# Kernel optimization log

Measured on AMD Instinct MI355X. Metric: run time of the kernel, lower is better.

## Reference

```python
import jax, jax.numpy as jnp
import numpy as np

N_LAYERS = 4
D_MODEL = 64        # 8*8 hardcoded in source
D_STATE = 128
D_CONV = 4
EXPAND = 2
HEADDIM = 64        # Mamba2Simple default
D_INNER = EXPAND * D_MODEL            # 128
NHEADS = D_INNER // HEADDIM           # 2
NGROUPS = 1
D_IN_PROJ = 2 * D_INNER + 2 * NGROUPS * D_STATE + NHEADS   # 514
CONV_DIM = D_INNER + 2 * NGROUPS * D_STATE                 # 384
EPS = 1e-5
B_SZ, SEQ = 8, 4096


def setup_inputs() -> dict:
    key = jax.random.key(0)
    ks = jax.random.split(key, 8)
    s = 0.02
    x = jax.random.normal(ks[0], (B_SZ, SEQ, D_MODEL), jnp.float32)
    in_proj_w = jax.random.normal(ks[1], (N_LAYERS, D_IN_PROJ, D_MODEL), jnp.float32) * s
    conv_w = jax.random.normal(ks[2], (N_LAYERS, CONV_DIM, 1, D_CONV), jnp.float32) * 0.2
    conv_b = jnp.zeros((N_LAYERS, CONV_DIM), jnp.float32)
    # dt_bias ~ inverse-softplus of small dt values
    dt_bias = jax.random.uniform(ks[3], (N_LAYERS, NHEADS), jnp.float32, -4.0, 0.0)
    A_log = jnp.log(jax.random.uniform(ks[4], (N_LAYERS, NHEADS), jnp.float32, 1.0, 16.0))
    D = jnp.ones((N_LAYERS, NHEADS), jnp.float32)
    norm_w = jnp.ones((N_LAYERS, D_INNER), jnp.float32)
    out_proj_w = jax.random.normal(ks[5], (N_LAYERS, D_MODEL, D_INNER), jnp.float32) * s
    return {"x": x, "in_proj_w": in_proj_w, "conv_w": conv_w, "conv_b": conv_b,
            "dt_bias": dt_bias, "A_log": A_log, "D": D, "norm_w": norm_w,
            "out_proj_w": out_proj_w}


def _ssm(xh, dt, A, Bm, Cm):
    """Selective-scan SSM. xh:(B,L,H,P) dt:(B,L,H) A:(H,) Bm,Cm:(B,L,S) -> (B,L,H,P)"""
    dA = jnp.exp(dt * A)  # (B,L,H)

    def step(h, inp):
        dA_t, dt_t, x_t, B_t, C_t = inp
        # h: (B,H,P,S)
        h = h * dA_t[:, :, None, None] + (dt_t[:, :, None] * x_t)[..., None] * B_t[:, None, None, :]
        y = jnp.einsum('bhps,bs->bhp', h, C_t)
        return h, y

    b = xh.shape[0]
    h0 = jnp.zeros((b, NHEADS, HEADDIM, D_STATE), xh.dtype)
    xs = (jnp.moveaxis(dA, 1, 0), jnp.moveaxis(dt, 1, 0), jnp.moveaxis(xh, 1, 0),
          jnp.moveaxis(Bm, 1, 0), jnp.moveaxis(Cm, 1, 0))
    _, ys = jax.lax.scan(step, h0, xs)
    return jnp.moveaxis(ys, 0, 1)


def _layer(x, p):
    in_w, cw, cb, dtb, Alog, Dp, nw, ow = p
    zxbcdt = x @ in_w.T                                   # (B,L,514)
    z = zxbcdt[..., :D_INNER]
    xBC = zxbcdt[..., D_INNER:D_INNER + CONV_DIM]
    dt = jax.nn.softplus(zxbcdt[..., -NHEADS:] + dtb)     # (B,L,H)
    # causal depthwise conv over sequence
    xc = jnp.moveaxis(xBC, -1, 1)                         # (B,C,L)
    xc = jax.lax.conv_general_dilated(xc, cw, (1,), [(D_CONV - 1, 0)],
                                      dimension_numbers=('NCH', 'OIH', 'NCH'),
                                      feature_group_count=CONV_DIM)
    xBC = jax.nn.silu(jnp.moveaxis(xc + cb[None, :, None], 1, -1))
    xs = xBC[..., :D_INNER]
    Bm = xBC[..., D_INNER:D_INNER + D_STATE]
    Cm = xBC[..., D_INNER + D_STATE:]
    xh = xs.reshape(xs.shape[0], xs.shape[1], NHEADS, HEADDIM)
    A = -jnp.exp(Alog)                                    # (H,)
    y = _ssm(xh, dt, A, Bm, Cm) + Dp[None, None, :, None] * xh
    y = y.reshape(y.shape[0], y.shape[1], D_INNER)
    # gated RMSNorm (norm_before_gate=False): rmsnorm(y * silu(z)) * w
    y = y * jax.nn.silu(z)
    y = y * jax.lax.rsqrt(jnp.mean(y * y, axis=-1, keepdims=True) + EPS) * nw
    return y @ ow.T


def reference(x, in_proj_w, conv_w, conv_b, dt_bias, A_log, D, norm_w, out_proj_w):
    def body(xc, p):
        return _layer(xc, p) + xc, None
    out, _ = jax.lax.scan(body, x, (in_proj_w, conv_w, conv_b, dt_bias, A_log, D, norm_w, out_proj_w))
    return out
```

## Files before the change

### kernel.cpp

```cpp
#include <hip/hip_runtime.h>
#include <math.h>

#define B_SZ 8
#define SEQ  4096
#define DM   64
#define DI   128
#define NH   2
#define HD   64
#define DS   128
#define DIP  514
#define ZW   512
#define CD   384
#define QC   64
#define NC   64
#define NR   (B_SZ*SEQ)
#define WPAD 576

typedef __attribute__((ext_vector_type(8))) short bf16x8;
typedef __attribute__((ext_vector_type(4))) float f32x4;

__device__ __forceinline__ unsigned short f2bf(float f) {
    union { float f; unsigned int u; } x; x.f = f;
    unsigned int r = x.u + 0x7fffu + ((x.u >> 16) & 1u);
    return (unsigned short)(r >> 16);
}
__device__ __forceinline__ float bf2f(unsigned short h) {
    union { unsigned int u; float f; } x; x.u = ((unsigned int)h) << 16;
    return x.f;
}
__device__ __forceinline__ bf16x8 fragld(const unsigned short* base, int r0, int k0, int ld) {
    int l = threadIdx.x & 63;
    return *(const bf16x8*)(base + (ptrdiff_t)(r0 + (l & 15)) * ld + k0 + (l >> 4) * 8);
}

__global__ __launch_bounds__(256) void k_wcvt(const float* __restrict__ in_w,
                                              const float* __restrict__ out_w,
                                              unsigned short* __restrict__ Wb,
                                              unsigned short* __restrict__ OWb) {
    int idx = blockIdx.x * 256 + threadIdx.x;
    if (idx < 4 * WPAD * 64) {
        int l = idx / (WPAD * 64), r = idx % (WPAD * 64);
        int n = r >> 6, k = r & 63;
        float v = (n < DIP) ? in_w[(size_t)l * DIP * 64 + (size_t)n * 64 + k] : 0.f;
        Wb[idx] = f2bf(v);
    }
    if (idx < 4 * 64 * 128) OWb[idx] = f2bf(out_w[idx]);
}

__global__ __launch_bounds__(256) void k_xcvt(const float* __restrict__ X,
                                              unsigned short* __restrict__ Xb) {
    int idx = (blockIdx.x * 256 + threadIdx.x) * 4;
    float4 v = *(const float4*)(X + idx);
    uint2 p;
    p.x = f2bf(v.x) | ((unsigned int)f2bf(v.y) << 16);
    p.y = f2bf(v.z) | ((unsigned int)f2bf(v.w) << 16);
    *(uint2*)(Xb + idx) = p;
}

__global__ __launch_bounds__(256) void k_inproj(const unsigned short* __restrict__ Xb,
                                                const unsigned short* __restrict__ Wb,
                                                unsigned short* __restrict__ ZXb,
                                                float* __restrict__ DT) {
    int m0 = blockIdx.x * 256;
    int n0 = blockIdx.y * 64;
    int tid = threadIdx.x;
    int wid = tid >> 6, lane = tid & 63;
    int q4 = lane >> 4, c16 = lane & 15;
    int mb = m0 + wid * 64;
    bf16x8 af[4][2];
#pragma unroll
    for (int mt = 0; mt < 4; mt++)
#pragma unroll
        for (int ks = 0; ks < 2; ks++)
            af[mt][ks] = *(const bf16x8*)(Xb + (size_t)(mb + mt * 16 + c16) * 64 + ks * 32 + q4 * 8);
    if (n0 < 512) {
#pragma unroll
        for (int nt = 0; nt < 4; nt++) {
            bf16x8 bf[2];
#pragma unroll
            for (int ks = 0; ks < 2; ks++)
                bf[ks] = *(const bf16x8*)(Wb + (size_t)(n0 + nt * 16 + c16) * 64 + ks * 32 + q4 * 8);
#pragma unroll
            for (int mt = 0; mt < 4; mt++) {
                f32x4 acc = {0.f, 0.f, 0.f, 0.f};
                acc = __builtin_amdgcn_mfma_f32_16x16x32_bf16(af[mt][0], bf[0], acc, 0, 0, 0);
                acc = __builtin_amdgcn_mfma_f32_16x16x32_bf16(af[mt][1], bf[1], acc, 0, 0, 0);
#pragma unroll
                for (int rr = 0; rr < 4; rr++) {
                    float v = acc[rr];
                    float vn = __shfl_xor(v, 1);
                    if (!(lane & 1)) {
                        unsigned int pk = f2bf(v) | ((unsigned int)f2bf(vn) << 16);
                        *(unsigned int*)(ZXb + (size_t)(mb + mt * 16 + q4 * 4 + rr) * ZW + n0 + nt * 16 + c16) = pk;
                    }
                }
            }
        }
    } else {
        bf16x8 bf[2];
#pragma unroll
        for (int ks = 0; ks < 2; ks++)
            bf[ks] = *(const bf16x8*)(Wb + (size_t)(512 + c16) * 64 + ks * 32 + q4 * 8);
#pragma unroll
        for (int mt = 0; mt < 4; mt++) {
            f32x4 acc = {0.f, 0.f, 0.f, 0.f};
            acc = __builtin_amdgcn_mfma_f32_16x16x32_bf16(af[mt][0], bf[0], acc, 0, 0, 0);
            acc = __builtin_amdgcn_mfma_f32_16x16x32_bf16(af[mt][1], bf[1], acc, 0, 0, 0);
            if (c16 < 2)
#pragma unroll
                for (int rr = 0; rr < 4; rr++)
                    DT[(size_t)(mb + mt * 16 + q4 * 4 + rr) * 2 + c16] = acc[rr];
        }
    }
}

__global__ __launch_bounds__(1024, 8) void k_chunk1(
        const unsigned short* __restrict__ ZXb, const float* __restrict__ DT,
        const float* __restrict__ CW, const float* __restrict__ CB,
        const float* __restrict__ dtb, const float* __restrict__ Alog,
        const float* __restrict__ Dv,
        unsigned short* __restrict__ SL, unsigned short* __restrict__ CBuf,
        float* __restrict__ EB,
        float* __restrict__ TB, unsigned short* __restrict__ YBb) {
    __shared__ unsigned short sBt[128][72];
    __shared__ unsigned short sXt[128][72];
    __shared__ unsigned short uBC[2][64][136];
    __shared__ float s_cum[2][64], s_dt[2][64], s_w[2][64];
    unsigned short (*sM)[64][72] = (unsigned short (*)[64][72])&uBC[0][0][0];

    int c = blockIdx.x, b = blockIdx.y;
    size_t rbase = (size_t)b * SEQ + c * QC;
    int tid = threadIdx.x;
    int wid = tid >> 6, lane = tid & 63;
    int q4 = lane >> 4, c16 = lane & 15;

    if (wid < 2) {
        int h = wid, j = lane;
        float raw = DT[(rbase + j) * 2 + h] + dtb[h];
        float dt = (raw > 20.f) ? raw : log1pf(__expf(raw));
        float A = -__expf(Alog[h]);
        float x = dt * A;
        for (int off = 1; off < 64; off <<= 1) {
            float o = __shfl_up(x, off);
            if (lane >= off) x += o;
        }
        float T = __shfl(x, 63);
        s_dt[h][j] = dt;
        s_cum[h][j] = x;
        s_w[h][j] = __expf(T - x) * dt;
        EB[((size_t)(b * NC + c)) * 128 + h * 64 + j] = __expf(x);
        if (j == 0) TB[(b * 2 + h) * NC + c] = __expf(T);
    }

    size_t cbbase = ((size_t)(b * NC + c)) * 8192;
    for (int e = tid; e < 64 * 96; e += 1024) {
        int j = e / 96;
        int q = e - j * 96;
        int cc = q * 4;
        int l = c * QC + j;
        const unsigned short* zp = ZXb + (rbase + j) * ZW + 128 + cc;
        uint2 a0 = *(const uint2*)zp;
        uint2 a1 = make_uint2(0, 0), a2 = make_uint2(0, 0), a3 = make_uint2(0, 0);
        if (l >= 1) a1 = *(const uint2*)(zp - ZW);
        if (l >= 2) a2 = *(const uint2*)(zp - 2 * ZW);
        if (l >= 3) a3 = *(const uint2*)(zp - 3 * ZW);
        float v[4];
#pragma unroll
        for (int u = 0; u < 4; u++) {
            unsigned int w0 = (u < 2) ? a0.x : a0.y;
            unsigned int w1 = (u < 2) ? a1.x : a1.y;
            unsigned int w2 = (u < 2) ? a2.x : a2.y;
            unsigned int w3 = (u < 2) ? a3.x : a3.y;
            int sh = (u & 1) * 16;
            float r0 = bf2f((unsigned short)(w0 >> sh));
            float r1 = bf2f((unsigned short)(w1 >> sh));
            float r2 = bf2f((unsigned short)(w2 >> sh));
            float r3 = bf2f((unsigned short)(w3 >> sh));
            float4 wv = *(const float4*)(CW + (cc + u) * 4);
            float tt = CB[cc + u] + wv.w * r0 + wv.z * r1 + wv.y * r2 + wv.x * r3;
            v[u] = tt / (1.f + __expf(-tt));
        }
        if (cc < 128) {
#pragma unroll
            for (int u = 0; u < 4; u++) sXt[cc + u][j] = f2bf(v[u]);
        } else if (cc < 256) {
            int s = cc - 128;
            unsigned int p0 = f2bf(v[0]) | ((unsigned int)f2bf(v[1]) << 16);
            unsigned int p1 = f2bf(v[2]) | ((unsigned int)f2bf(v[3]) << 16);
            *(uint2*)&uBC[0][j][s] = make_uint2(p0, p1);
#pragma unroll
            for (int u = 0; u < 4; u++) sBt[s + u][j] = f2bf(v[u]);
        } else {
            int s = cc - 256;
            unsigned int p0 = f2bf(v[0]) | ((unsigned int)f2bf(v[1]) << 16);
            unsigned int p1 = f2bf(v[2]) | ((unsigned int)f2bf(v[3]) << 16);
            *(uint2*)&uBC[1][j][s] = make_uint2(p0, p1);
            *(uint2*)(CBuf + cbbase + (size_t)j * 128 + s) = make_uint2(p0, p1);
        }
    }
    __syncthreads();

    f32x4 gacc;
    {
        int it = wid >> 2, jt = wid & 3;
        f32x4 acc = {0.f, 0.f, 0.f, 0.f};
        for (int ks = 0; ks < 4; ks++) {
            bf16x8 a = fragld(&uBC[1][0][0], it * 16, ks * 32, 136);
            bf16x8 bb = fragld(&uBC[0][0][0], jt * 16, ks * 32, 136);
            acc = __builtin_amdgcn_mfma_f32_16x16x32_bf16(a, bb, acc, 0, 0, 0);
        }
        gacc = acc;
    }
    __syncthreads();
    {
        int it = wid >> 2, jt = wid & 3;
        int j = jt * 16 + c16;
        for (int rr = 0; rr < 4; rr++) {
            int i = it * 16 + q4 * 4 + rr;
            float gv = gacc[rr];
            for (int h = 0; h < 2; h++) {
                float m = 0.f;
                if (j <= i) m = gv * __expf(s_cum[h][i] - s_cum[h][j]) * s_dt[h][j];
                sM[h][i][j] = f2bf(m);
            }
        }
    }
    __syncthreads();

#pragma unroll
    for (int u = 0; u < 2; u++) {
        int idx = wid * 2 + u;
        int h = idx >> 4, tt = idx & 15;
        int it = tt >> 2, pt = tt & 3;
        float dco = Dv[h];
        int pg = h * 64 + pt * 16 + c16;
        f32x4 acc;
        for (int rr = 0; rr < 4; rr++) {
            int i = it * 16 + q4 * 4 + rr;
            acc[rr] = dco * bf2f(sXt[pg][i]);
        }
        for (int ks = 0; ks < 2; ks++) {
            bf16x8 a = fragld(&sM[h][0][0], it * 16, ks * 32, 72);
            bf16x8 bb = fragld(&sXt[0][0], h * 64 + pt * 16, ks * 32, 72);
            acc = __builtin_amdgcn_mfma_f32_16x16x32_bf16(a, bb, acc, 0, 0, 0);
        }
        for (int rr = 0; rr < 4; rr++) {
            int i = it * 16 + q4 * 4 + rr;
            float v = acc[rr];
            float vn = __shfl_xor(v, 1);
            if (!(lane & 1)) {
                unsigned int pk = f2bf(v) | ((unsigned int)f2bf(vn) << 16);
                *(unsigned int*)(YBb + (rbase + i) * DI + pg) = pk;
            }
        }
    }
    size_t slbase = ((size_t)(b * NC + c)) * 16384;
#pragma unroll
    for (int u = 0; u < 4; u++) {
        int idx = wid * 4 + u;
        int ptl = idx >> 3, st = idx & 7;
        int h = ptl >> 2;
        f32x4 acc = {0.f, 0.f, 0.f, 0.f};
        for (int ks = 0; ks < 2; ks++) {
            int jb = ks * 32 + (lane >> 4) * 8;
            bf16x8 a = fragld(&sXt[0][0], ptl * 16, ks * 32, 72);
            bf16x8 aw;
#pragma unroll
            for (int t = 0; t < 8; t++) aw[t] = (short)f2bf(bf2f((unsigned short)a[t]) * s_w[h][jb + t]);
            bf16x8 bb = fragld(&sBt[0][0], st * 16, ks * 32, 72);
            acc = __builtin_amdgcn_mfma_f32_16x16x32_bf16(aw, bb, acc, 0, 0, 0);
        }
        int s = st * 16 + c16;
        for (int rr = 0; rr < 4; rr++) {
            int p = ptl * 16 + q4 * 4 + rr;
            float vv = acc[rr];
            float vn = __shfl_xor(vv, 1);
            if (!(lane & 1)) {
                unsigned int pk = f2bf(vv) | ((unsigned int)f2bf(vn) << 16);
                *(unsigned int*)(SL + slbase + (size_t)p * 128 + s) = pk;
            }
        }
    }
}

__global__ __launch_bounds__(128) void k_scan(unsigned short* __restrict__ SL,
                                              const float* __restrict__ TB) {
    int bid = blockIdx.x;
    int b = bid >> 5;
    int ps = ((bid & 31) * 128 + threadIdx.x) * 4;
    int h = ps >> 13;
    const float* dAp = TB + (b * 2 + h) * NC;
    size_t base = (size_t)(b * NC) * 16384 + ps;
    float h0 = 0.f, h1 = 0.f, h2 = 0.f, h3 = 0.f;
    uint2 cur = *(const uint2*)(SL + base);
    for (int cc = 0; cc < NC; cc++) {
        uint2 nxt = make_uint2(0, 0);
        if (cc + 1 < NC) nxt = *(const uint2*)(SL + base + (size_t)(cc + 1) * 16384);
        float dA = dAp[cc];
        float s0 = bf2f((unsigned short)(cur.x & 0xffff));
        float s1 = bf2f((unsigned short)(cur.x >> 16));
        float s2 = bf2f((unsigned short)(cur.y & 0xffff));
        float s3 = bf2f((unsigned short)(cur.y >> 16));
        uint2 st;
        st.x = f2bf(h0) | ((unsigned int)f2bf(h1) << 16);
        st.y = f2bf(h2) | ((unsigned int)f2bf(h3) << 16);
        *(uint2*)(SL + base + (size_t)cc * 16384) = st;
        h0 = h0 * dA + s0;
        h1 = h1 * dA + s1;
        h2 = h2 * dA + s2;
        h3 = h3 * dA + s3;
        cur = nxt;
    }
}

__global__ __launch_bounds__(1024, 8) void k_fused(
        const unsigned short* __restrict__ SL, const unsigned short* __restrict__ CBuf,
        const float* __restrict__ EB,
        const unsigned short* __restrict__ YBb, const unsigned short* __restrict__ ZXb,
        const float* __restrict__ NW, const unsigned short* __restrict__ OWb,
        unsigned short* __restrict__ Xb, float* __restrict__ OutF, int last) {
    __shared__ __attribute__((aligned(16))) unsigned short sH[128][136];
    __shared__ __attribute__((aligned(16))) unsigned short sE[128][136];
    float* sGf = (float*)&sH[0][0];
    unsigned short (*sG)[136] = (unsigned short (*)[136])&sE[0][0];

    int c = blockIdx.x, b = blockIdx.y;
    size_t rbase = (size_t)b * SEQ + c * QC;
    int tid = threadIdx.x;
    int wid = tid >> 6, lane = tid & 63;
    size_t base = ((size_t)(b * NC + c)) * 16384;
    for (int u = 0; u < 2; u++) {
        int e = u * 1024 + tid;
        int row = e >> 4, cb8 = (e & 15) * 8;
        *(uint4*)&sH[row][cb8] = *(const uint4*)(SL + base + (size_t)row * 128 + cb8);
    }
    size_t cbbase = ((size_t)(b * NC + c)) * 8192;
    size_t ebase  = ((size_t)(b * NC + c)) * 128;
    {
        int i = tid >> 4, sc = (tid & 15) * 8;
        uint4 cv = *(const uint4*)(CBuf + cbbase + (size_t)i * 128 + sc);
        float e0 = EB[ebase + i], e1 = EB[ebase + 64 + i];
        unsigned int w[4] = {cv.x, cv.y, cv.z, cv.w};
        uint4 o0, o1;
        unsigned int* po0 = &o0.x;
        unsigned int* po1 = &o1.x;
#pragma unroll
        for (int t = 0; t < 4; t++) {
            float lo = bf2f((unsigned short)(w[t] & 0xffff));
            float hi = bf2f((unsigned short)(w[t] >> 16));
            po0[t] = f2bf(lo * e0) | ((unsigned int)f2bf(hi * e0) << 16);
            po1[t] = f2bf(lo * e1) | ((unsigned int)f2bf(hi * e1) << 16);
        }
        *(uint4*)&sE[i][sc] = o0;
        *(uint4*)&sE[64 + i][sc] = o1;
    }
    __syncthreads();
    int q4 = lane >> 4, c16 = lane & 15;

    float yv[2][4];
    int tit[2], tpg[2];
#pragma unroll
    for (int u = 0; u < 2; u++) {
        int idx = wid * 2 + u;
        int h = idx >> 4, tt = idx & 15;
        int it = tt >> 2, pt = tt & 3;
        f32x4 acc = {0.f, 0.f, 0.f, 0.f};
        for (int ks = 0; ks < 4; ks++) {
            bf16x8 a = fragld(&sE[0][0], h * 64 + it * 16, ks * 32, 136);
            bf16x8 bb = fragld(&sH[0][0], h * 64 + pt * 16, ks * 32, 136);
            acc = __builtin_amdgcn_mfma_f32_16x16x32_bf16(a, bb, acc, 0, 0, 0);
        }
        int pg = h * 64 + pt * 16 + c16;
        tit[u] = it; tpg[u] = pg;
        for (int rr = 0; rr < 4; rr++) {
            int i = it * 16 + q4 * 4 + rr;
            float y = acc[rr] + bf2f(YBb[(rbase + i) * DI + pg]);
            float z = bf2f(ZXb[(rbase + i) * ZW + pg]);
            yv[u][rr] = y * (z / (1.f + __expf(-z)));
        }
    }
    __syncthreads();
#pragma unroll
    for (int u = 0; u < 2; u++)
        for (int rr = 0; rr < 4; rr++) {
            int i = tit[u] * 16 + q4 * 4 + rr;
            sGf[i * 132 + tpg[u]] = yv[u][rr];
        }
    __syncthreads();
    {
        int row = tid >> 4, part = tid & 15;
        int d0 = part * 8;
        float g[8];
        float ss = 0.f;
        for (int t2 = 0; t2 < 8; t2++) { g[t2] = sGf[row * 132 + d0 + t2]; ss += g[t2] * g[t2]; }
        ss += __shfl_xor(ss, 1);
        ss += __shfl_xor(ss, 2);
        ss += __shfl_xor(ss, 4);
        ss += __shfl_xor(ss, 8);
        float rms = rsqrtf(ss * (1.f / 128.f) + 1e-5f);
        for (int t2 = 0; t2 < 8; t2 += 2) {
            unsigned int pk = f2bf(g[t2] * rms * NW[d0 + t2]) |
                              ((unsigned int)f2bf(g[t2 + 1] * rms * NW[d0 + t2 + 1]) << 16);
            *(unsigned int*)&sG[row][d0 + t2] = pk;
        }
    }
    __syncthreads();
    {
        int mt = wid >> 2, nt = wid & 3;
        f32x4 acc = {0.f, 0.f, 0.f, 0.f};
        for (int ks = 0; ks < 4; ks++) {
            bf16x8 a = fragld(&sG[0][0], mt * 16, ks * 32, 136);
            bf16x8 bb = *(const bf16x8*)(OWb + (size_t)(nt * 16 + c16) * 128 + ks * 32 + q4 * 8);
            acc = __builtin_amdgcn_mfma_f32_16x16x32_bf16(a, bb, acc, 0, 0, 0);
        }
        for (int rr = 0; rr < 4; rr++) {
            int m = mt * 16 + q4 * 4 + rr;
            int n = nt * 16 + c16;
            size_t o = (rbase + m) * DM + n;
            float v = bf2f(Xb[o]) + acc[rr];
            if (last) {
                OutF[o] = v;
            } else {
                float vn = __shfl_xor(v, 1);
                if (!(lane & 1)) {
                    unsigned int pk = f2bf(v) | ((unsigned int)f2bf(vn) << 16);
                    *(unsigned int*)(Xb + o) = pk;
                }
            }
        }
    }
}

extern "C" void kernel_launch(void* const* d_in, const int* in_sizes, int n_in,
                              void* d_out, int out_size, void* d_ws, size_t ws_size,
                              hipStream_t stream) {
    const float* x       = (const float*)d_in[0];
    const float* in_w    = (const float*)d_in[1];
    const float* conv_w  = (const float*)d_in[2];
    const float* conv_b  = (const float*)d_in[3];
    const float* dt_bias = (const float*)d_in[4];
    const float* A_log   = (const float*)d_in[5];
    const float* Dp      = (const float*)d_in[6];
    const float* norm_w  = (const float*)d_in[7];
    const float* out_w   = (const float*)d_in[8];
    float* out = (float*)d_out;
    float* ws  = (float*)d_ws;

    float* dt = ws;
    float* tb = dt + (size_t)NR * 2;
    float* eb = tb + 1024;
    unsigned short* zxb  = (unsigned short*)(eb + (size_t)B_SZ * NC * 128);
    unsigned short* ybb  = zxb + (size_t)NR * ZW;
    unsigned short* sl   = ybb + (size_t)NR * DI;
    unsigned short* cbuf = sl + (size_t)B_SZ * NC * 16384;
    unsigned short* xb   = cbuf + (size_t)B_SZ * NC * 8192;
    unsigned short* wb   = xb + (size_t)NR * DM;
    unsigned short* owb  = wb + (size_t)4 * WPAD * 64;

    k_wcvt<<<(4 * WPAD * 64 + 255) / 256, 256, 0, stream>>>(in_w, out_w, wb, owb);
    k_xcvt<<<NR * DM / 1024, 256, 0, stream>>>(x, xb);

    for (int layer = 0; layer < 4; layer++) {
        k_inproj<<<dim3(NR / 256, 9), 256, 0, stream>>>(xb, wb + (size_t)layer * WPAD * 64, zxb, dt);
        k_chunk1<<<dim3(NC, B_SZ), 1024, 0, stream>>>(zxb, dt,
                conv_w + (size_t)layer * CD * 4, conv_b + (size_t)layer * CD,
                dt_bias + layer * NH, A_log + layer * NH, Dp + layer * NH,
                sl, cbuf, eb, tb, ybb);
        k_scan<<<256, 128, 0, stream>>>(sl, tb);
        k_fused<<<dim3(NC, B_SZ), 1024, 0, stream>>>(sl, cbuf, eb, ybb,
                zxb, norm_w + layer * DI, owb + (size_t)layer * 64 * 128, xb, out,
                (layer == 3) ? 1 : 0);
    }
}
```

Baseline: 389.1 us.

## Recompute z gate in fused kernel instead of storing it; simplify scan

The in-projection no longer writes the z columns to the intermediate buffer. The buffer shrinks from 512 to 384 columns and the launch grid drops from 9 to 7 column tiles. The fused output kernel instead recomputes z with a small MFMA over the bf16 activations and the z rows of the weight matrix, trading a little extra compute for less global write and read traffic. The chunk-state scan is also rewritten to process one element per thread with 256-thread blocks and a partially unrolled loop, replacing the four-element, software-prefetched version.

```diff
diff --git a/kernel.cpp b/kernel.cpp
--- a/kernel.cpp
+++ b/kernel.cpp
@@ -9,7 +9,7 @@
 #define HD   64
 #define DS   128
 #define DIP  514
-#define ZW   512
+#define XW   384
 #define CD   384
 #define QC   64
 #define NC   64
@@ -62,7 +62,7 @@
                                                 unsigned short* __restrict__ ZXb,
                                                 float* __restrict__ DT) {
     int m0 = blockIdx.x * 256;
-    int n0 = blockIdx.y * 64;
+    int ny = blockIdx.y;
     int tid = threadIdx.x;
     int wid = tid >> 6, lane = tid & 63;
     int q4 = lane >> 4, c16 = lane & 15;
@@ -73,13 +73,13 @@
 #pragma unroll
         for (int ks = 0; ks < 2; ks++)
             af[mt][ks] = *(const bf16x8*)(Xb + (size_t)(mb + mt * 16 + c16) * 64 + ks * 32 + q4 * 8);
-    if (n0 < 512) {
+    if (ny < 6) {
 #pragma unroll
         for (int nt = 0; nt < 4; nt++) {
             bf16x8 bf[2];
 #pragma unroll
             for (int ks = 0; ks < 2; ks++)
-                bf[ks] = *(const bf16x8*)(Wb + (size_t)(n0 + nt * 16 + c16) * 64 + ks * 32 + q4 * 8);
+                bf[ks] = *(const bf16x8*)(Wb + (size_t)(128 + ny * 64 + nt * 16 + c16) * 64 + ks * 32 + q4 * 8);
 #pragma unroll
             for (int mt = 0; mt < 4; mt++) {
                 f32x4 acc = {0.f, 0.f, 0.f, 0.f};
@@ -91,7 +91,7 @@
                     float vn = __shfl_xor(v, 1);
                     if (!(lane & 1)) {
                         unsigned int pk = f2bf(v) | ((unsigned int)f2bf(vn) << 16);
-                        *(unsigned int*)(ZXb + (size_t)(mb + mt * 16 + q4 * 4 + rr) * ZW + n0 + nt * 16 + c16) = pk;
+                        *(unsigned int*)(ZXb + (size_t)(mb + mt * 16 + q4 * 4 + rr) * XW + ny * 64 + nt * 16 + c16) = pk;
                     }
                 }
             }
@@ -158,12 +158,12 @@
         int q = e - j * 96;
         int cc = q * 4;
         int l = c * QC + j;
-        const unsigned short* zp = ZXb + (rbase + j) * ZW + 128 + cc;
+        const unsigned short* zp = ZXb + (rbase + j) * XW + cc;
         uint2 a0 = *(const uint2*)zp;
         uint2 a1 = make_uint2(0, 0), a2 = make_uint2(0, 0), a3 = make_uint2(0, 0);
-        if (l >= 1) a1 = *(const uint2*)(zp - ZW);
-        if (l >= 2) a2 = *(const uint2*)(zp - 2 * ZW);
-        if (l >= 3) a3 = *(const uint2*)(zp - 3 * ZW);
+        if (l >= 1) a1 = *(const uint2*)(zp - XW);
+        if (l >= 2) a2 = *(const uint2*)(zp - 2 * XW);
+        if (l >= 3) a3 = *(const uint2*)(zp - 3 * XW);
         float v[4];
 #pragma unroll
         for (int u = 0; u < 4; u++) {
@@ -283,40 +283,28 @@
     }
 }
 
-__global__ __launch_bounds__(128) void k_scan(unsigned short* __restrict__ SL,
+__global__ __launch_bounds__(256) void k_scan(unsigned short* __restrict__ SL,
                                               const float* __restrict__ TB) {
     int bid = blockIdx.x;
-    int b = bid >> 5;
-    int ps = ((bid & 31) * 128 + threadIdx.x) * 4;
+    int b = bid >> 6;
+    int ps = (bid & 63) * 256 + threadIdx.x;
     int h = ps >> 13;
     const float* dAp = TB + (b * 2 + h) * NC;
     size_t base = (size_t)(b * NC) * 16384 + ps;
-    float h0 = 0.f, h1 = 0.f, h2 = 0.f, h3 = 0.f;
-    uint2 cur = *(const uint2*)(SL + base);
+    float hacc = 0.f;
+#pragma unroll 8
     for (int cc = 0; cc < NC; cc++) {
-        uint2 nxt = make_uint2(0, 0);
-        if (cc + 1 < NC) nxt = *(const uint2*)(SL + base + (size_t)(cc + 1) * 16384);
-        float dA = dAp[cc];
-        float s0 = bf2f((unsigned short)(cur.x & 0xffff));
-        float s1 = bf2f((unsigned short)(cur.x >> 16));
-        float s2 = bf2f((unsigned short)(cur.y & 0xffff));
-        float s3 = bf2f((unsigned short)(cur.y >> 16));
-        uint2 st;
-        st.x = f2bf(h0) | ((unsigned int)f2bf(h1) << 16);
-        st.y = f2bf(h2) | ((unsigned int)f2bf(h3) << 16);
-        *(uint2*)(SL + base + (size_t)cc * 16384) = st;
-        h0 = h0 * dA + s0;
-        h1 = h1 * dA + s1;
-        h2 = h2 * dA + s2;
-        h3 = h3 * dA + s3;
-        cur = nxt;
+        size_t idx = base + (size_t)cc * 16384;
+        float slv = bf2f(SL[idx]);
+        SL[idx] = f2bf(hacc);
+        hacc = hacc * dAp[cc] + slv;
     }
 }
 
 __global__ __launch_bounds__(1024, 8) void k_fused(
         const unsigned short* __restrict__ SL, const unsigned short* __restrict__ CBuf,
         const float* __restrict__ EB,
-        const unsigned short* __restrict__ YBb, const unsigned short* __restrict__ ZXb,
+        const unsigned short* __restrict__ YBb, const unsigned short* __restrict__ Wzb,
         const float* __restrict__ NW, const unsigned short* __restrict__ OWb,
         unsigned short* __restrict__ Xb, float* __restrict__ OutF, int last) {
     __shared__ __attribute__((aligned(16))) unsigned short sH[128][136];
@@ -364,18 +352,25 @@
         int idx = wid * 2 + u;
         int h = idx >> 4, tt = idx & 15;
         int it = tt >> 2, pt = tt & 3;
+        int pg = h * 64 + pt * 16 + c16;
+        f32x4 zacc = {0.f, 0.f, 0.f, 0.f};
         f32x4 acc = {0.f, 0.f, 0.f, 0.f};
+#pragma unroll
+        for (int ks = 0; ks < 2; ks++) {
+            bf16x8 xa = fragld(Xb, (int)rbase + it * 16, ks * 32, 64);
+            bf16x8 wz = fragld(Wzb, h * 64 + pt * 16, ks * 32, 64);
+            zacc = __builtin_amdgcn_mfma_f32_16x16x32_bf16(xa, wz, zacc, 0, 0, 0);
+        }
         for (int ks = 0; ks < 4; ks++) {
             bf16x8 a = fragld(&sE[0][0], h * 64 + it * 16, ks * 32, 136);
             bf16x8 bb = fragld(&sH[0][0], h * 64 + pt * 16, ks * 32, 136);
             acc = __builtin_amdgcn_mfma_f32_16x16x32_bf16(a, bb, acc, 0, 0, 0);
         }
-        int pg = h * 64 + pt * 16 + c16;
         tit[u] = it; tpg[u] = pg;
         for (int rr = 0; rr < 4; rr++) {
             int i = it * 16 + q4 * 4 + rr;
             float y = acc[rr] + bf2f(YBb[(rbase + i) * DI + pg]);
-            float z = bf2f(ZXb[(rbase + i) * ZW + pg]);
+            float z = zacc[rr];
             yv[u][rr] = y * (z / (1.f + __expf(-z)));
         }
     }
@@ -450,7 +445,7 @@
     float* tb = dt + (size_t)NR * 2;
     float* eb = tb + 1024;
     unsigned short* zxb  = (unsigned short*)(eb + (size_t)B_SZ * NC * 128);
-    unsigned short* ybb  = zxb + (size_t)NR * ZW;
+    unsigned short* ybb  = zxb + (size_t)NR * XW;
     unsigned short* sl   = ybb + (size_t)NR * DI;
     unsigned short* cbuf = sl + (size_t)B_SZ * NC * 16384;
     unsigned short* xb   = cbuf + (size_t)B_SZ * NC * 8192;
@@ -461,14 +456,15 @@
     k_xcvt<<<NR * DM / 1024, 256, 0, stream>>>(x, xb);
 
     for (int layer = 0; layer < 4; layer++) {
-        k_inproj<<<dim3(NR / 256, 9), 256, 0, stream>>>(xb, wb + (size_t)layer * WPAD * 64, zxb, dt);
+        k_inproj<<<dim3(NR / 256, 7), 256, 0, stream>>>(xb, wb + (size_t)layer * WPAD * 64, zxb, dt);
         k_chunk1<<<dim3(NC, B_SZ), 1024, 0, stream>>>(zxb, dt,
                 conv_w + (size_t)layer * CD * 4, conv_b + (size_t)layer * CD,
                 dt_bias + layer * NH, A_log + layer * NH, Dp + layer * NH,
                 sl, cbuf, eb, tb, ybb);
-        k_scan<<<256, 128, 0, stream>>>(sl, tb);
+        k_scan<<<512, 256, 0, stream>>>(sl, tb);
         k_fused<<<dim3(NC, B_SZ), 1024, 0, stream>>>(sl, cbuf, eb, ybb,
-                zxb, norm_w + layer * DI, owb + (size_t)layer * 64 * 128, xb, out,
+                wb + (size_t)layer * WPAD * 64, norm_w + layer * DI,
+                owb + (size_t)layer * 64 * 128, xb, out,
                 (layer == 3) ? 1 : 0);
     }
 }
```

After: 357.8 us. -8.0%, faster.
